# Kernel tuning notes

Hardware: AMD Instinct MI355X
Metric: run time of the kernel (lower is better)

Reference implementation:

```python
import jax, jax.numpy as jnp
import numpy as np
import math

# dims: batch, tgt len, enc len, embed, heads, layers, ffn, vocab, text dim, image dim, gate hidden
B, T, S, E, H, L, F, V, DT, DI, GH = 16, 200, 100, 256, 8, 2, 1024, 50000, 768, 512, 64
NEG = -1e9

PARAM_SHAPES = [
    ("item_emb", (V, E)), ("pos_emb", (T, E)),
    ("sa_qkv_w", (L, E, 3 * E)), ("sa_qkv_b", (L, 3 * E)), ("sa_out_w", (L, E, E)), ("sa_out_b", (L, E)),
    ("ca_qkv_w", (L, E, 3 * E)), ("ca_qkv_b", (L, 3 * E)), ("ca_out_w", (L, E, E)), ("ca_out_b", (L, E)),
    ("n1_s", (L, E)), ("n1_b", (L, E)), ("n2_s", (L, E)), ("n2_b", (L, E)), ("n3_s", (L, E)), ("n3_b", (L, E)),
    ("ffn_w1", (L, E, F)), ("ffn_b1", (L, F)), ("ffn_w2", (L, F, E)), ("ffn_b2", (L, E)),
    ("g_w1", (E, GH)), ("g_b1", (GH,)), ("g_w2", (GH, 3)), ("g_b2", (3,)),
    ("be_w", (E, E)), ("be_b", (E,)),
    ("text_mat", (V, DT)), ("tp_w", (DT, E)), ("tp_b", (E,)),
    ("ct_qkv_w", (E, 3 * E)), ("ct_qkv_b", (3 * E,)), ("ct_out_w", (E, E)), ("ct_out_b", (E,)),
    ("ce_w1", (E, 2 * E)), ("ce_b1", (2 * E,)), ("ce_w2", (2 * E, E)), ("ce_b2", (E,)),
    ("img_mat", (V, DI)), ("ip_w", (DI, E)), ("ip_b", (E,)),
    ("im_qkv_w", (E, 3 * E)), ("im_qkv_b", (3 * E,)), ("im_out_w", (E, E)), ("im_out_b", (E,)),
    ("ie_w1", (E, 2 * E)), ("ie_b1", (2 * E,)), ("ie_w2", (2 * E, E)), ("ie_b2", (E,)),
    ("fin_w", (E, V)), ("fin_b", (V,)),
]


def setup_inputs() -> dict:
    keys = iter(jax.random.split(jax.random.key(0), 80))
    d = {}
    d["target_ids"] = jax.random.randint(next(keys), (B, T), 0, V)
    d["encoder_output"] = jax.random.normal(next(keys), (B, S, E), dtype=jnp.float32)
    d["memory_padding_mask"] = jax.random.randint(next(keys), (B, S), 0, 2) == 1
    for name, shape in PARAM_SHAPES:
        d[name] = jax.random.normal(next(keys), shape, dtype=jnp.float32) * 0.02
    for n in ("n1_s", "n2_s", "n3_s"):
        d[n] = jnp.ones((L, E), jnp.float32)  # LayerNorm gains init to 1
    d["item_emb"] = d["item_emb"].at[0].set(0.0)  # padding_idx=0
    return d


def _ln(x, s, b, eps=1e-5):
    mu = jnp.mean(x, axis=-1, keepdims=True)
    var = jnp.mean(jnp.square(x - mu), axis=-1, keepdims=True)
    return (x - mu) / jnp.sqrt(var + eps) * s + b


def _mha(xq, xkv, wqkv, bqkv, wout, bout, bias):
    # torch nn.MultiheadAttention (batch_first): joint QKV proj, H heads, out proj
    Bq, Tq, _ = xq.shape
    Tk = xkv.shape[1]
    wq, wk, wv = jnp.split(wqkv, 3, axis=1)
    bq, bk, bv = jnp.split(bqkv, 3)
    Dh = E // H
    q = (xq @ wq + bq).reshape(Bq, Tq, H, Dh)
    k = (xkv @ wk + bk).reshape(Bq, Tk, H, Dh)
    v = (xkv @ wv + bv).reshape(Bq, Tk, H, Dh)
    logits = jnp.einsum("bthd,bshd->bhts", q, k) / math.sqrt(Dh)
    if bias is not None:
        logits = logits + bias
    a = jax.nn.softmax(logits, axis=-1)
    ctx = jnp.einsum("bhts,bshd->bthd", a, v).reshape(Bq, Tq, E)
    return ctx @ wout + bout


def reference(target_ids, encoder_output, memory_padding_mask, item_emb, pos_emb,
              sa_qkv_w, sa_qkv_b, sa_out_w, sa_out_b, ca_qkv_w, ca_qkv_b, ca_out_w, ca_out_b,
              n1_s, n1_b, n2_s, n2_b, n3_s, n3_b, ffn_w1, ffn_b1, ffn_w2, ffn_b2,
              g_w1, g_b1, g_w2, g_b2, be_w, be_b,
              text_mat, tp_w, tp_b, ct_qkv_w, ct_qkv_b, ct_out_w, ct_out_b, ce_w1, ce_b1, ce_w2, ce_b2,
              img_mat, ip_w, ip_b, im_qkv_w, im_qkv_b, im_out_w, im_out_b, ie_w1, ie_b1, ie_w2, ie_b2,
              fin_w, fin_b):
    causal = jnp.where(jnp.tril(jnp.ones((T, T), bool)), 0.0, -jnp.inf)[None, None]  # [1,1,T,T]
    pad_bias = jnp.where(memory_padding_mask[:, None, None, :], NEG, 0.0)  # [B,1,1,S]
    x = item_emb[target_ids] * math.sqrt(E) + pos_emb[None]  # [B,T,E]
    for l in range(L):
        x = _ln(x + _mha(x, x, sa_qkv_w[l], sa_qkv_b[l], sa_out_w[l], sa_out_b[l], causal), n1_s[l], n1_b[l])
        x = _ln(x + _mha(x, encoder_output, ca_qkv_w[l], ca_qkv_b[l], ca_out_w[l], ca_out_b[l], pad_bias), n2_s[l], n2_b[l])
        h = jax.nn.relu(x @ ffn_w1[l] + ffn_b1[l]) @ ffn_w2[l] + ffn_b2[l]
        x = _ln(x + h, n3_s[l], n3_b[l])
    # softmax gate over 3 experts (eval: no noise)
    gate = jax.nn.softmax(jax.nn.relu(x @ g_w1 + g_b1) @ g_w2 + g_b2, axis=-1)  # [B,T,3]
    e_beh = x @ be_w + be_b
    th = text_mat[target_ids] @ tp_w + tp_b
    cctx = _mha(x, th, ct_qkv_w, ct_qkv_b, ct_out_w, ct_out_b, None)
    e_txt = jax.nn.relu(cctx @ ce_w1 + ce_b1) @ ce_w2 + ce_b2
    ih = img_mat[target_ids] @ ip_w + ip_b
    ictx = _mha(x, ih, im_qkv_w, im_qkv_b, im_out_w, im_out_b, None)
    e_img = jax.nn.relu(ictx @ ie_w1 + ie_b1) @ ie_w2 + ie_b2
    hfin = gate[..., 0:1] * e_beh + gate[..., 1:2] * e_txt + gate[..., 2:3] * e_img  # [B,T,E]
    return hfin @ fin_w + fin_b  # [B,T,V] full-vocab logits
```

## Files before the change

### kernel.cpp

```cpp
#include <hip/hip_runtime.h>
#include <cstdint>
#include <cstddef>

#define BB 16
#define TT 200
#define SS 100
#define EE 256
#define HH 8
#define LL 2
#define FF 1024
#define VV 50000
#define DTXT 768
#define DIMG 512
#define GHH 64
#define MROWS (BB * TT)
#define MENC  (BB * SS)

using bf16x8 = __attribute__((ext_vector_type(8))) short;
using f32x4  = __attribute__((ext_vector_type(4))) float;

__device__ __forceinline__ short f2bf(float f) {
    unsigned u = __float_as_uint(f);
    u += 0x7fffu + ((u >> 16) & 1u);
    return (short)(u >> 16);
}

__global__ __launch_bounds__(256)
void k_transpose_bf16(const float* __restrict__ in, short* __restrict__ out, int K, int N) {
    __shared__ float tile[32][33];
    int n0 = blockIdx.x * 32, k0 = blockIdx.y * 32;
    for (int i = threadIdx.y; i < 32; i += 8) {
        int k = k0 + i, n = n0 + threadIdx.x;
        tile[i][threadIdx.x] = (k < K && n < N) ? in[(size_t)k * N + n] : 0.f;
    }
    __syncthreads();
    for (int i = threadIdx.y; i < 32; i += 8) {
        int n = n0 + i, k = k0 + threadIdx.x;
        if (n < N && k < K) out[(size_t)n * K + k] = f2bf(tile[threadIdx.x][i]);
    }
}

__global__ __launch_bounds__(256)
void k_gemm_bf16(const float* __restrict__ A, int lda, const int* __restrict__ aidx,
                 const short* __restrict__ Bt, const float* __restrict__ bias,
                 float* __restrict__ C, int ldc, int M, int N, int K, int dorelu) {
    int tid  = threadIdx.x;
    int wave = tid >> 6, lane = tid & 63;
    int lr = lane & 15, lq = lane >> 4;
    int m_base = blockIdx.y * 128 + (wave >> 1) * 64;
    int n_base = blockIdx.x * 128 + (wave & 1) * 64;

    const float* arow[4];
    const short* brow[4];
#pragma unroll
    for (int mt = 0; mt < 4; ++mt) {
        int m = m_base + mt * 16 + lr;
        if (m >= M) m = M - 1;
        int r = aidx ? aidx[m] : m;
        arow[mt] = A + (size_t)r * lda + lq * 8;
    }
#pragma unroll
    for (int nt = 0; nt < 4; ++nt) {
        int n = n_base + nt * 16 + lr;
        if (n >= N) n = N - 1;
        brow[nt] = Bt + (size_t)n * K + lq * 8;
    }

    f32x4 acc[4][4];
#pragma unroll
    for (int a = 0; a < 4; ++a)
#pragma unroll
        for (int b = 0; b < 4; ++b)
#pragma unroll
            for (int i = 0; i < 4; ++i) acc[a][b][i] = 0.f;

    for (int k0 = 0; k0 < K; k0 += 32) {
        bf16x8 af[4], bfr[4];
#pragma unroll
        for (int mt = 0; mt < 4; ++mt) {
            const float4* p = (const float4*)(arow[mt] + k0);
            float4 u = p[0], v = p[1];
            bf16x8 t;
            t[0] = f2bf(u.x); t[1] = f2bf(u.y); t[2] = f2bf(u.z); t[3] = f2bf(u.w);
            t[4] = f2bf(v.x); t[5] = f2bf(v.y); t[6] = f2bf(v.z); t[7] = f2bf(v.w);
            af[mt] = t;
        }
#pragma unroll
        for (int nt = 0; nt < 4; ++nt)
            bfr[nt] = *(const bf16x8*)(brow[nt] + k0);
#pragma unroll
        for (int mt = 0; mt < 4; ++mt)
#pragma unroll
            for (int nt = 0; nt < 4; ++nt)
                acc[mt][nt] = __builtin_amdgcn_mfma_f32_16x16x32_bf16(af[mt], bfr[nt], acc[mt][nt], 0, 0, 0);
    }

#pragma unroll
    for (int mt = 0; mt < 4; ++mt)
#pragma unroll
        for (int nt = 0; nt < 4; ++nt) {
            int col = n_base + nt * 16 + lr;
            if (col >= N) continue;
            float bv = bias ? bias[col] : 0.f;
#pragma unroll
            for (int i = 0; i < 4; ++i) {
                int row = m_base + mt * 16 + lq * 4 + i;
                if (row >= M) continue;
                float v = acc[mt][nt][i] + bv;
                if (dorelu) v = fmaxf(v, 0.f);
                C[(size_t)row * ldc + col] = v;
            }
        }
}

template <int MODE>
__global__ __launch_bounds__(256)
void k_attn(const float* __restrict__ q, int qld,
            const float* __restrict__ k, const float* __restrict__ v, int kvld,
            const int* __restrict__ mask,
            float* __restrict__ out, int T, int Tk) {
    int b = blockIdx.z, h = blockIdx.y;
    int t = threadIdx.x;
    __shared__ float kl[TT][32];
    __shared__ float vl[TT][32];
    for (int idx = threadIdx.x; idx < Tk * 32; idx += 256) {
        int s = idx >> 5, i = idx & 31;
        kl[s][i] = k[((size_t)b * Tk + s) * kvld + h * 32 + i];
        vl[s][i] = v[((size_t)b * Tk + s) * kvld + h * 32 + i];
    }
    __syncthreads();
    if (t >= T) return;

    float qv[32];
    const float* qp = q + ((size_t)b * T + t) * qld + h * 32;
#pragma unroll
    for (int i = 0; i < 32; ++i) qv[i] = qp[i];

    float m = -INFINITY, l = 0.f, ctx[32];
#pragma unroll
    for (int i = 0; i < 32; ++i) ctx[i] = 0.f;

    int send = (MODE == 1) ? (t + 1) : Tk;
    for (int s = 0; s < send; ++s) {
        float d = 0.f;
#pragma unroll
        for (int i = 0; i < 32; ++i) d += qv[i] * kl[s][i];
        d *= 0.17677669529663687f;
        if (MODE == 2) { if (mask[b * Tk + s]) d += -1e9f; }
        if (d > m) {
            float f = __expf(m - d);
            l *= f;
#pragma unroll
            for (int i = 0; i < 32; ++i) ctx[i] *= f;
            m = d;
        }
        float p = __expf(d - m);
        l += p;
#pragma unroll
        for (int i = 0; i < 32; ++i) ctx[i] += p * vl[s][i];
    }
    float inv = 1.f / l;
    float* op = out + ((size_t)b * T + t) * EE + h * 32;
#pragma unroll
    for (int i = 0; i < 32; ++i) op[i] = ctx[i] * inv;
}

__global__ __launch_bounds__(256)
void k_ln_res(const float* __restrict__ a, const float* __restrict__ bres,
              const float* __restrict__ gain, const float* __restrict__ beta,
              float* __restrict__ out) {
    int row = blockIdx.x, i = threadIdx.x;
    __shared__ float red[256];
    float x = a[(size_t)row * EE + i] + bres[(size_t)row * EE + i];
    red[i] = x;
    __syncthreads();
    for (int s = 128; s > 0; s >>= 1) { if (i < s) red[i] += red[i + s]; __syncthreads(); }
    float mu = red[0] * (1.f / EE);
    __syncthreads();
    float d = x - mu;
    red[i] = d * d;
    __syncthreads();
    for (int s = 128; s > 0; s >>= 1) { if (i < s) red[i] += red[i + s]; __syncthreads(); }
    float var = red[0] * (1.f / EE);
    float r = rsqrtf(var + 1e-5f);
    out[(size_t)row * EE + i] = d * r * gain[i] + beta[i];
}

__global__ __launch_bounds__(64)
void k_gate(const float* __restrict__ x, const float* __restrict__ w1, const float* __restrict__ b1,
            const float* __restrict__ w2, const float* __restrict__ b2, float* __restrict__ gate) {
    int row = blockIdx.x, j = threadIdx.x;
    __shared__ float xr[EE];
    __shared__ float hr[GHH];
    for (int i = j; i < EE; i += 64) xr[i] = x[(size_t)row * EE + i];
    __syncthreads();
    float acc = b1[j];
    for (int i = 0; i < EE; ++i) acc += xr[i] * w1[i * GHH + j];
    hr[j] = fmaxf(acc, 0.f);
    __syncthreads();
    if (j == 0) {
        float g[3];
        for (int c = 0; c < 3; ++c) {
            float a = b2[c];
            for (int kk = 0; kk < GHH; ++kk) a += hr[kk] * w2[kk * 3 + c];
            g[c] = a;
        }
        float mx = fmaxf(g[0], fmaxf(g[1], g[2]));
        float e0 = __expf(g[0] - mx), e1 = __expf(g[1] - mx), e2 = __expf(g[2] - mx);
        float inv = 1.f / (e0 + e1 + e2);
        gate[(size_t)row * 3 + 0] = e0 * inv;
        gate[(size_t)row * 3 + 1] = e1 * inv;
        gate[(size_t)row * 3 + 2] = e2 * inv;
    }
}

__global__ __launch_bounds__(256)
void k_embed(const int* __restrict__ ids, const float* __restrict__ item,
             const float* __restrict__ pos, float* __restrict__ out) {
    int idx = blockIdx.x * 256 + threadIdx.x;
    if (idx >= MROWS * EE) return;
    int bt = idx >> 8, e = idx & 255;
    int t = bt % TT;
    out[idx] = item[(size_t)ids[bt] * EE + e] * 16.f + pos[t * EE + e];
}

__global__ __launch_bounds__(256)
void k_combine(const float* __restrict__ g, const float* __restrict__ e0,
               const float* __restrict__ e1, const float* __restrict__ e2,
               float* __restrict__ out) {
    int idx = blockIdx.x * 256 + threadIdx.x;
    if (idx >= MROWS * EE) return;
    int row = idx >> 8;
    out[idx] = g[(size_t)row * 3] * e0[idx] + g[(size_t)row * 3 + 1] * e1[idx] + g[(size_t)row * 3 + 2] * e2[idx];
}

extern "C" void kernel_launch(void* const* d_in, const int* in_sizes, int n_in,
                              void* d_out, int out_size, void* d_ws, size_t ws_size,
                              hipStream_t stream) {
    (void)in_sizes; (void)n_in; (void)out_size; (void)ws_size;

    const int*   ids      = (const int*)d_in[0];
    const float* enc      = (const float*)d_in[1];
    const int*   mask     = (const int*)d_in[2];
    const float* item_emb = (const float*)d_in[3];
    const float* pos_emb  = (const float*)d_in[4];
    const float* sa_qkv_w = (const float*)d_in[5];
    const float* sa_qkv_b = (const float*)d_in[6];
    const float* sa_out_w = (const float*)d_in[7];
    const float* sa_out_b = (const float*)d_in[8];
    const float* ca_qkv_w = (const float*)d_in[9];
    const float* ca_qkv_b = (const float*)d_in[10];
    const float* ca_out_w = (const float*)d_in[11];
    const float* ca_out_b = (const float*)d_in[12];
    const float* n1_s = (const float*)d_in[13];
    const float* n1_b = (const float*)d_in[14];
    const float* n2_s = (const float*)d_in[15];
    const float* n2_b = (const float*)d_in[16];
    const float* n3_s = (const float*)d_in[17];
    const float* n3_b = (const float*)d_in[18];
    const float* ffn_w1 = (const float*)d_in[19];
    const float* ffn_b1 = (const float*)d_in[20];
    const float* ffn_w2 = (const float*)d_in[21];
    const float* ffn_b2 = (const float*)d_in[22];
    const float* g_w1 = (const float*)d_in[23];
    const float* g_b1 = (const float*)d_in[24];
    const float* g_w2 = (const float*)d_in[25];
    const float* g_b2 = (const float*)d_in[26];
    const float* be_w = (const float*)d_in[27];
    const float* be_b = (const float*)d_in[28];
    const float* text_mat = (const float*)d_in[29];
    const float* tp_w = (const float*)d_in[30];
    const float* tp_b = (const float*)d_in[31];
    const float* ct_qkv_w = (const float*)d_in[32];
    const float* ct_qkv_b = (const float*)d_in[33];
    const float* ct_out_w = (const float*)d_in[34];
    const float* ct_out_b = (const float*)d_in[35];
    const float* ce_w1 = (const float*)d_in[36];
    const float* ce_b1 = (const float*)d_in[37];
    const float* ce_w2 = (const float*)d_in[38];
    const float* ce_b2 = (const float*)d_in[39];
    const float* img_mat = (const float*)d_in[40];
    const float* ip_w = (const float*)d_in[41];
    const float* ip_b = (const float*)d_in[42];
    const float* im_qkv_w = (const float*)d_in[43];
    const float* im_qkv_b = (const float*)d_in[44];
    const float* im_out_w = (const float*)d_in[45];
    const float* im_out_b = (const float*)d_in[46];
    const float* ie_w1 = (const float*)d_in[47];
    const float* ie_b1 = (const float*)d_in[48];
    const float* ie_w2 = (const float*)d_in[49];
    const float* ie_b2 = (const float*)d_in[50];
    const float* fin_w = (const float*)d_in[51];
    const float* fin_b = (const float*)d_in[52];
    float* out = (float*)d_out;

    char* pws = (char*)d_ws;
    auto alloc = [&](size_t bytes) -> void* {
        void* r = (void*)pws;
        pws += (bytes + 255) & ~(size_t)255;
        return r;
    };
    short* wsaqkv = (short*)alloc((size_t)LL * 768 * 256 * 2);
    short* wsaout = (short*)alloc((size_t)LL * 256 * 256 * 2);
    short* wcaqkv = (short*)alloc((size_t)LL * 768 * 256 * 2);
    short* wcaout = (short*)alloc((size_t)LL * 256 * 256 * 2);
    short* wffn1  = (short*)alloc((size_t)LL * 1024 * 256 * 2);
    short* wffn2  = (short*)alloc((size_t)LL * 256 * 1024 * 2);
    short* wbe    = (short*)alloc((size_t)256 * 256 * 2);
    short* wtp    = (short*)alloc((size_t)256 * 768 * 2);
    short* wctqkv = (short*)alloc((size_t)768 * 256 * 2);
    short* wctout = (short*)alloc((size_t)256 * 256 * 2);
    short* wce1   = (short*)alloc((size_t)512 * 256 * 2);
    short* wce2   = (short*)alloc((size_t)256 * 512 * 2);
    short* wip    = (short*)alloc((size_t)256 * 512 * 2);
    short* wimqkv = (short*)alloc((size_t)768 * 256 * 2);
    short* wimout = (short*)alloc((size_t)256 * 256 * 2);
    short* wie1   = (short*)alloc((size_t)512 * 256 * 2);
    short* wie2   = (short*)alloc((size_t)256 * 512 * 2);
    short* wfin   = (short*)alloc((size_t)VV * 256 * 2);

    float* xbuf   = (float*)alloc((size_t)MROWS * 256 * 4);
    float* qkvbuf = (float*)alloc((size_t)MROWS * 768 * 4);
    float* qbuf   = (float*)alloc((size_t)MROWS * 256 * 4);
    float* kvbuf  = (float*)alloc((size_t)MROWS * 512 * 4);
    float* ctxbuf = (float*)alloc((size_t)MROWS * 256 * 4);
    float* obuf   = (float*)alloc((size_t)MROWS * 256 * 4);
    float* pbuf   = (float*)alloc((size_t)MROWS * 1024 * 4);
    float* thbuf  = (float*)alloc((size_t)MROWS * 256 * 4);
    float* gatebuf= (float*)alloc((size_t)MROWS * 4 * 4);
    float* ebeh   = (float*)alloc((size_t)MROWS * 256 * 4);
    float* etxt   = (float*)alloc((size_t)MROWS * 256 * 4);
    float* eimg   = (float*)alloc((size_t)MROWS * 256 * 4);
    float* hfin   = (float*)alloc((size_t)MROWS * 256 * 4);

    auto tr = [&](const float* in, short* o, int K, int N) {
        dim3 g((N + 31) / 32, (K + 31) / 32);
        k_transpose_bf16<<<g, dim3(32, 8), 0, stream>>>(in, o, K, N);
    };
    auto gemm = [&](const float* A, int lda, const int* aidx, const short* Bt,
                    const float* bias, float* C, int ldc, int M, int N, int K, int relu) {
        dim3 g((N + 127) / 128, (M + 127) / 128);
        k_gemm_bf16<<<g, 256, 0, stream>>>(A, lda, aidx, Bt, bias, C, ldc, M, N, K, relu);
    };
    auto attn = [&](int mode, const float* q, int qld, const float* k, const float* v,
                    int kvld, const int* mk, float* o, int Tk) {
        dim3 g(1, HH, BB);
        if (mode == 0)      k_attn<0><<<g, 256, 0, stream>>>(q, qld, k, v, kvld, mk, o, TT, Tk);
        else if (mode == 1) k_attn<1><<<g, 256, 0, stream>>>(q, qld, k, v, kvld, mk, o, TT, Tk);
        else                k_attn<2><<<g, 256, 0, stream>>>(q, qld, k, v, kvld, mk, o, TT, Tk);
    };
    auto ln = [&](const float* a, const float* b, const float* gain, const float* beta, float* o) {
        k_ln_res<<<MROWS, 256, 0, stream>>>(a, b, gain, beta, o);
    };

    for (int l = 0; l < LL; ++l) {
        tr(sa_qkv_w + (size_t)l * 256 * 768, wsaqkv + (size_t)l * 768 * 256, 256, 768);
        tr(sa_out_w + (size_t)l * 256 * 256, wsaout + (size_t)l * 256 * 256, 256, 256);
        tr(ca_qkv_w + (size_t)l * 256 * 768, wcaqkv + (size_t)l * 768 * 256, 256, 768);
        tr(ca_out_w + (size_t)l * 256 * 256, wcaout + (size_t)l * 256 * 256, 256, 256);
        tr(ffn_w1 + (size_t)l * 256 * 1024, wffn1 + (size_t)l * 1024 * 256, 256, 1024);
        tr(ffn_w2 + (size_t)l * 1024 * 256, wffn2 + (size_t)l * 256 * 1024, 1024, 256);
    }
    tr(be_w, wbe, 256, 256);
    tr(tp_w, wtp, 768, 256);
    tr(ct_qkv_w, wctqkv, 256, 768);
    tr(ct_out_w, wctout, 256, 256);
    tr(ce_w1, wce1, 256, 512);
    tr(ce_w2, wce2, 512, 256);
    tr(ip_w, wip, 512, 256);
    tr(im_qkv_w, wimqkv, 256, 768);
    tr(im_out_w, wimout, 256, 256);
    tr(ie_w1, wie1, 256, 512);
    tr(ie_w2, wie2, 512, 256);
    tr(fin_w, wfin, 256, VV);

    k_embed<<<(MROWS * EE + 255) / 256, 256, 0, stream>>>(ids, item_emb, pos_emb, xbuf);

    for (int l = 0; l < LL; ++l) {
        gemm(xbuf, 256, nullptr, wsaqkv + (size_t)l * 768 * 256, sa_qkv_b + (size_t)l * 768,
             qkvbuf, 768, MROWS, 768, 256, 0);
        attn(1, qkvbuf, 768, qkvbuf + 256, qkvbuf + 512, 768, nullptr, ctxbuf, TT);
        gemm(ctxbuf, 256, nullptr, wsaout + (size_t)l * 256 * 256, sa_out_b + (size_t)l * 256,
             obuf, 256, MROWS, 256, 256, 0);
        ln(xbuf, obuf, n1_s + (size_t)l * 256, n1_b + (size_t)l * 256, xbuf);
        gemm(xbuf, 256, nullptr, wcaqkv + (size_t)l * 768 * 256, ca_qkv_b + (size_t)l * 768,
             qbuf, 256, MROWS, 256, 256, 0);
        gemm(enc, 256, nullptr, wcaqkv + (size_t)l * 768 * 256 + 256 * 256,
             ca_qkv_b + (size_t)l * 768 + 256, kvbuf, 512, MENC, 512, 256, 0);
        attn(2, qbuf, 256, kvbuf, kvbuf + 256, 512, mask, ctxbuf, SS);
        gemm(ctxbuf, 256, nullptr, wcaout + (size_t)l * 256 * 256, ca_out_b + (size_t)l * 256,
             obuf, 256, MROWS, 256, 256, 0);
        ln(xbuf, obuf, n2_s + (size_t)l * 256, n2_b + (size_t)l * 256, xbuf);
        gemm(xbuf, 256, nullptr, wffn1 + (size_t)l * 1024 * 256, ffn_b1 + (size_t)l * 1024,
             pbuf, 1024, MROWS, 1024, 256, 1);
        gemm(pbuf, 1024, nullptr, wffn2 + (size_t)l * 256 * 1024, ffn_b2 + (size_t)l * 256,
             obuf, 256, MROWS, 256, 1024, 0);
        ln(xbuf, obuf, n3_s + (size_t)l * 256, n3_b + (size_t)l * 256, xbuf);
    }

    k_gate<<<MROWS, 64, 0, stream>>>(xbuf, g_w1, g_b1, g_w2, g_b2, gatebuf);
    gemm(xbuf, 256, nullptr, wbe, be_b, ebeh, 256, MROWS, 256, 256, 0);

    gemm(text_mat, DTXT, ids, wtp, tp_b, thbuf, 256, MROWS, 256, DTXT, 0);
    gemm(xbuf, 256, nullptr, wctqkv, ct_qkv_b, qbuf, 256, MROWS, 256, 256, 0);
    gemm(thbuf, 256, nullptr, wctqkv + 256 * 256, ct_qkv_b + 256, kvbuf, 512, MROWS, 512, 256, 0);
    attn(0, qbuf, 256, kvbuf, kvbuf + 256, 512, nullptr, ctxbuf, TT);
    gemm(ctxbuf, 256, nullptr, wctout, ct_out_b, obuf, 256, MROWS, 256, 256, 0);
    gemm(obuf, 256, nullptr, wce1, ce_b1, pbuf, 512, MROWS, 512, 256, 1);
    gemm(pbuf, 512, nullptr, wce2, ce_b2, etxt, 256, MROWS, 256, 512, 0);

    gemm(img_mat, DIMG, ids, wip, ip_b, thbuf, 256, MROWS, 256, DIMG, 0);
    gemm(xbuf, 256, nullptr, wimqkv, im_qkv_b, qbuf, 256, MROWS, 256, 256, 0);
    gemm(thbuf, 256, nullptr, wimqkv + 256 * 256, im_qkv_b + 256, kvbuf, 512, MROWS, 512, 256, 0);
    attn(0, qbuf, 256, kvbuf, kvbuf + 256, 512, nullptr, ctxbuf, TT);
    gemm(ctxbuf, 256, nullptr, wimout, im_out_b, obuf, 256, MROWS, 256, 256, 0);
    gemm(obuf, 256, nullptr, wie1, ie_b1, pbuf, 512, MROWS, 512, 256, 1);
    gemm(pbuf, 512, nullptr, wie2, ie_b2, eimg, 256, MROWS, 256, 512, 0);

    k_combine<<<(MROWS * EE + 255) / 256, 256, 0, stream>>>(gatebuf, ebeh, etxt, eimg, hfin);
    gemm(hfin, 256, nullptr, wfin, fin_b, out, VV, MROWS, VV, 256, 0);
}
```

Measured before the change: 2.544 ms.

## Stage bf16 GEMM operands through LDS with double-buffered direct loads

Rewrites the GEMM to take bf16 A operands and stage 128x64 A/B tiles into LDS with global_load_lds, double-buffered across K steps. Producers (layernorm, embed, attention, combine, GEMM epilogues) now emit bf16 copies, and the encoder, text and image gathers are pre-cast to bf16 rows. The aim is to cut global traffic and the fp32->bf16 conversion inside the GEMM inner loop, and to overlap loads with MFMA. The cost is extra bf16 buffers and cast kernels, and intermediates are rounded to bf16. The loop assumes K is a multiple of 64.

```diff
diff --git a/kernel.cpp b/kernel.cpp
--- a/kernel.cpp
+++ b/kernel.cpp
@@ -41,30 +41,60 @@
 }
 
 __global__ __launch_bounds__(256)
-void k_gemm_bf16(const float* __restrict__ A, int lda, const int* __restrict__ aidx,
-                 const short* __restrict__ Bt, const float* __restrict__ bias,
-                 float* __restrict__ C, int ldc, int M, int N, int K, int dorelu) {
+void k_cast_rows(const float* __restrict__ in, int ldin, const int* __restrict__ idx,
+                 short* __restrict__ out, int cols) {
+    int r = blockIdx.x;
+    int src = idx ? idx[r] : r;
+    const float4* ip = (const float4*)(in + (size_t)src * ldin);
+    short* op = out + (size_t)r * cols;
+    for (int j = threadIdx.x; j * 4 < cols; j += blockDim.x) {
+        float4 u = ip[j];
+        short4 s;
+        s.x = f2bf(u.x); s.y = f2bf(u.y); s.z = f2bf(u.z); s.w = f2bf(u.w);
+        *(short4*)(op + j * 4) = s;
+    }
+}
+
+__global__ __launch_bounds__(256, 2)
+void k_gemm_bf16(const short* __restrict__ A, int lda,
+                 const short* __restrict__ Bt, int ldb,
+                 const float* __restrict__ bias,
+                 float* __restrict__ C, short* __restrict__ Cb, int ldc,
+                 int M, int N, int K, int dorelu) {
+    __shared__ short lsa[2][8][128][8];
+    __shared__ short lsb[2][8][128][8];
     int tid  = threadIdx.x;
     int wave = tid >> 6, lane = tid & 63;
     int lr = lane & 15, lq = lane >> 4;
-    int m_base = blockIdx.y * 128 + (wave >> 1) * 64;
-    int n_base = blockIdx.x * 128 + (wave & 1) * 64;
-
-    const float* arow[4];
-    const short* brow[4];
-#pragma unroll
-    for (int mt = 0; mt < 4; ++mt) {
-        int m = m_base + mt * 16 + lr;
-        if (m >= M) m = M - 1;
-        int r = aidx ? aidx[m] : m;
-        arow[mt] = A + (size_t)r * lda + lq * 8;
-    }
-#pragma unroll
-    for (int nt = 0; nt < 4; ++nt) {
-        int n = n_base + nt * 16 + lr;
-        if (n >= N) n = N - 1;
-        brow[nt] = Bt + (size_t)n * K + lq * 8;
-    }
+    int wm = (wave >> 1) * 64, wn = (wave & 1) * 64;
+    int mblk = blockIdx.y * 128, nblk = blockIdx.x * 128;
+
+    const short* pA[4];
+    const short* pB[4];
+#pragma unroll
+    for (int i = 0; i < 4; ++i) {
+        int c = wave * 4 + i;
+        int kg = c >> 1, half = (c & 1) * 64;
+        int ra = mblk + half + lane; if (ra > M - 1) ra = M - 1;
+        int rb = nblk + half + lane; if (rb > N - 1) rb = N - 1;
+        pA[i] = A  + (size_t)ra * lda + kg * 8;
+        pB[i] = Bt + (size_t)rb * ldb + kg * 8;
+    }
+
+    auto stage = [&](int buf) {
+#pragma unroll
+        for (int i = 0; i < 4; ++i) {
+            int c = wave * 4 + i;
+            int kg = c >> 1, half = (c & 1) * 64;
+            __builtin_amdgcn_global_load_lds(
+                (const __attribute__((address_space(1))) void*)pA[i],
+                (__attribute__((address_space(3))) void*)&lsa[buf][kg][half][0], 16, 0, 0);
+            __builtin_amdgcn_global_load_lds(
+                (const __attribute__((address_space(1))) void*)pB[i],
+                (__attribute__((address_space(3))) void*)&lsb[buf][kg][half][0], 16, 0, 0);
+            pA[i] += 64; pB[i] += 64;
+        }
+    };
 
     f32x4 acc[4][4];
 #pragma unroll
@@ -74,41 +104,47 @@
 #pragma unroll
             for (int i = 0; i < 4; ++i) acc[a][b][i] = 0.f;
 
-    for (int k0 = 0; k0 < K; k0 += 32) {
-        bf16x8 af[4], bfr[4];
-#pragma unroll
-        for (int mt = 0; mt < 4; ++mt) {
-            const float4* p = (const float4*)(arow[mt] + k0);
-            float4 u = p[0], v = p[1];
-            bf16x8 t;
-            t[0] = f2bf(u.x); t[1] = f2bf(u.y); t[2] = f2bf(u.z); t[3] = f2bf(u.w);
-            t[4] = f2bf(v.x); t[5] = f2bf(v.y); t[6] = f2bf(v.z); t[7] = f2bf(v.w);
-            af[mt] = t;
-        }
-#pragma unroll
-        for (int nt = 0; nt < 4; ++nt)
-            bfr[nt] = *(const bf16x8*)(brow[nt] + k0);
-#pragma unroll
-        for (int mt = 0; mt < 4; ++mt)
-#pragma unroll
-            for (int nt = 0; nt < 4; ++nt)
-                acc[mt][nt] = __builtin_amdgcn_mfma_f32_16x16x32_bf16(af[mt], bfr[nt], acc[mt][nt], 0, 0, 0);
+    stage(0);
+    __syncthreads();
+
+    int nk = K >> 6;
+    for (int kt = 0; kt < nk; ++kt) {
+        int cur = kt & 1;
+        if (kt + 1 < nk) stage(cur ^ 1);
+        bf16x8 af[2][4], bfr[2][4];
+#pragma unroll
+        for (int kk = 0; kk < 2; ++kk)
+#pragma unroll
+            for (int t = 0; t < 4; ++t) {
+                af[kk][t]  = *(const bf16x8*)&lsa[cur][kk * 4 + lq][wm + t * 16 + lr][0];
+                bfr[kk][t] = *(const bf16x8*)&lsb[cur][kk * 4 + lq][wn + t * 16 + lr][0];
+            }
+#pragma unroll
+        for (int kk = 0; kk < 2; ++kk)
+#pragma unroll
+            for (int mt = 0; mt < 4; ++mt)
+#pragma unroll
+                for (int nt = 0; nt < 4; ++nt)
+                    acc[mt][nt] = __builtin_amdgcn_mfma_f32_16x16x32_bf16(
+                        af[kk][mt], bfr[kk][nt], acc[mt][nt], 0, 0, 0);
+        __syncthreads();
     }
 
 #pragma unroll
     for (int mt = 0; mt < 4; ++mt)
 #pragma unroll
         for (int nt = 0; nt < 4; ++nt) {
-            int col = n_base + nt * 16 + lr;
+            int col = nblk + wn + nt * 16 + lr;
             if (col >= N) continue;
             float bv = bias ? bias[col] : 0.f;
 #pragma unroll
             for (int i = 0; i < 4; ++i) {
-                int row = m_base + mt * 16 + lq * 4 + i;
+                int row = mblk + wm + mt * 16 + lq * 4 + i;
                 if (row >= M) continue;
                 float v = acc[mt][nt][i] + bv;
                 if (dorelu) v = fmaxf(v, 0.f);
-                C[(size_t)row * ldc + col] = v;
+                if (C)  C[(size_t)row * ldc + col]  = v;
+                if (Cb) Cb[(size_t)row * ldc + col] = f2bf(v);
             }
         }
 }
@@ -118,7 +154,7 @@
 void k_attn(const float* __restrict__ q, int qld,
             const float* __restrict__ k, const float* __restrict__ v, int kvld,
             const int* __restrict__ mask,
-            float* __restrict__ out, int T, int Tk) {
+            short* __restrict__ out, int T, int Tk) {
     int b = blockIdx.z, h = blockIdx.y;
     int t = threadIdx.x;
     __shared__ float kl[TT][32];
@@ -160,15 +196,15 @@
         for (int i = 0; i < 32; ++i) ctx[i] += p * vl[s][i];
     }
     float inv = 1.f / l;
-    float* op = out + ((size_t)b * T + t) * EE + h * 32;
-#pragma unroll
-    for (int i = 0; i < 32; ++i) op[i] = ctx[i] * inv;
+    short* op = out + ((size_t)b * T + t) * EE + h * 32;
+#pragma unroll
+    for (int i = 0; i < 32; ++i) op[i] = f2bf(ctx[i] * inv);
 }
 
 __global__ __launch_bounds__(256)
 void k_ln_res(const float* __restrict__ a, const float* __restrict__ bres,
               const float* __restrict__ gain, const float* __restrict__ beta,
-              float* __restrict__ out) {
+              float* __restrict__ out, short* __restrict__ ob) {
     int row = blockIdx.x, i = threadIdx.x;
     __shared__ float red[256];
     float x = a[(size_t)row * EE + i] + bres[(size_t)row * EE + i];
@@ -183,7 +219,9 @@
     for (int s = 128; s > 0; s >>= 1) { if (i < s) red[i] += red[i + s]; __syncthreads(); }
     float var = red[0] * (1.f / EE);
     float r = rsqrtf(var + 1e-5f);
-    out[(size_t)row * EE + i] = d * r * gain[i] + beta[i];
+    float y = d * r * gain[i] + beta[i];
+    out[(size_t)row * EE + i] = y;
+    ob[(size_t)row * EE + i] = f2bf(y);
 }
 
 __global__ __launch_bounds__(64)
@@ -216,22 +254,26 @@
 
 __global__ __launch_bounds__(256)
 void k_embed(const int* __restrict__ ids, const float* __restrict__ item,
-             const float* __restrict__ pos, float* __restrict__ out) {
+             const float* __restrict__ pos, float* __restrict__ out,
+             short* __restrict__ xb) {
     int idx = blockIdx.x * 256 + threadIdx.x;
     if (idx >= MROWS * EE) return;
     int bt = idx >> 8, e = idx & 255;
     int t = bt % TT;
-    out[idx] = item[(size_t)ids[bt] * EE + e] * 16.f + pos[t * EE + e];
+    float v = item[(size_t)ids[bt] * EE + e] * 16.f + pos[t * EE + e];
+    out[idx] = v;
+    xb[idx] = f2bf(v);
 }
 
 __global__ __launch_bounds__(256)
 void k_combine(const float* __restrict__ g, const float* __restrict__ e0,
                const float* __restrict__ e1, const float* __restrict__ e2,
-               float* __restrict__ out) {
+               short* __restrict__ out) {
     int idx = blockIdx.x * 256 + threadIdx.x;
     if (idx >= MROWS * EE) return;
     int row = idx >> 8;
-    out[idx] = g[(size_t)row * 3] * e0[idx] + g[(size_t)row * 3 + 1] * e1[idx] + g[(size_t)row * 3 + 2] * e2[idx];
+    float v = g[(size_t)row * 3] * e0[idx] + g[(size_t)row * 3 + 1] * e1[idx] + g[(size_t)row * 3 + 2] * e2[idx];
+    out[idx] = f2bf(v);
 }
 
 extern "C" void kernel_launch(void* const* d_in, const int* in_sizes, int n_in,
@@ -323,34 +365,40 @@
     float* qkvbuf = (float*)alloc((size_t)MROWS * 768 * 4);
     float* qbuf   = (float*)alloc((size_t)MROWS * 256 * 4);
     float* kvbuf  = (float*)alloc((size_t)MROWS * 512 * 4);
-    float* ctxbuf = (float*)alloc((size_t)MROWS * 256 * 4);
     float* obuf   = (float*)alloc((size_t)MROWS * 256 * 4);
-    float* pbuf   = (float*)alloc((size_t)MROWS * 1024 * 4);
-    float* thbuf  = (float*)alloc((size_t)MROWS * 256 * 4);
     float* gatebuf= (float*)alloc((size_t)MROWS * 4 * 4);
     float* ebeh   = (float*)alloc((size_t)MROWS * 256 * 4);
     float* etxt   = (float*)alloc((size_t)MROWS * 256 * 4);
     float* eimg   = (float*)alloc((size_t)MROWS * 256 * 4);
-    float* hfin   = (float*)alloc((size_t)MROWS * 256 * 4);
+    short* xb     = (short*)alloc((size_t)MROWS * 256 * 2);
+    short* encb   = (short*)alloc((size_t)MENC * 256 * 2);
+    short* ctxb   = (short*)alloc((size_t)MROWS * 256 * 2);
+    short* pbh    = (short*)alloc((size_t)MROWS * 1024 * 2);
+    short* thb    = (short*)alloc((size_t)MROWS * 256 * 2);
+    short* obb    = (short*)alloc((size_t)MROWS * 256 * 2);
+    short* hfb    = (short*)alloc((size_t)MROWS * 256 * 2);
+    short* tg     = (short*)alloc((size_t)MROWS * 768 * 2);
+    short* ig     = (short*)alloc((size_t)MROWS * 512 * 2);
 
     auto tr = [&](const float* in, short* o, int K, int N) {
         dim3 g((N + 31) / 32, (K + 31) / 32);
         k_transpose_bf16<<<g, dim3(32, 8), 0, stream>>>(in, o, K, N);
     };
-    auto gemm = [&](const float* A, int lda, const int* aidx, const short* Bt,
-                    const float* bias, float* C, int ldc, int M, int N, int K, int relu) {
+    auto gemm = [&](const short* A, int lda, const short* Bt, const float* bias,
+                    float* C, short* Cb, int ldc, int M, int N, int K, int relu) {
         dim3 g((N + 127) / 128, (M + 127) / 128);
-        k_gemm_bf16<<<g, 256, 0, stream>>>(A, lda, aidx, Bt, bias, C, ldc, M, N, K, relu);
+        k_gemm_bf16<<<g, 256, 0, stream>>>(A, lda, Bt, K, bias, C, Cb, ldc, M, N, K, relu);
     };
     auto attn = [&](int mode, const float* q, int qld, const float* k, const float* v,
-                    int kvld, const int* mk, float* o, int Tk) {
+                    int kvld, const int* mk, short* o, int Tk) {
         dim3 g(1, HH, BB);
         if (mode == 0)      k_attn<0><<<g, 256, 0, stream>>>(q, qld, k, v, kvld, mk, o, TT, Tk);
         else if (mode == 1) k_attn<1><<<g, 256, 0, stream>>>(q, qld, k, v, kvld, mk, o, TT, Tk);
         else                k_attn<2><<<g, 256, 0, stream>>>(q, qld, k, v, kvld, mk, o, TT, Tk);
     };
-    auto ln = [&](const float* a, const float* b, const float* gain, const float* beta, float* o) {
-        k_ln_res<<<MROWS, 256, 0, stream>>>(a, b, gain, beta, o);
+    auto ln = [&](const float* a, const float* b, const float* gain, const float* beta,
+                  float* o, short* ob) {
+        k_ln_res<<<MROWS, 256, 0, stream>>>(a, b, gain, beta, o, ob);
     };
 
     for (int l = 0; l < LL; ++l) {
@@ -374,49 +422,53 @@
     tr(ie_w2, wie2, 512, 256);
     tr(fin_w, wfin, 256, VV);
 
-    k_embed<<<(MROWS * EE + 255) / 256, 256, 0, stream>>>(ids, item_emb, pos_emb, xbuf);
+    k_cast_rows<<<MENC, 64, 0, stream>>>(enc, 256, nullptr, encb, 256);
+    k_cast_rows<<<MROWS, 192, 0, stream>>>(text_mat, DTXT, ids, tg, DTXT);
+    k_cast_rows<<<MROWS, 128, 0, stream>>>(img_mat, DIMG, ids, ig, DIMG);
+
+    k_embed<<<(MROWS * EE + 255) / 256, 256, 0, stream>>>(ids, item_emb, pos_emb, xbuf, xb);
 
     for (int l = 0; l < LL; ++l) {
-        gemm(xbuf, 256, nullptr, wsaqkv + (size_t)l * 768 * 256, sa_qkv_b + (size_t)l * 768,
-             qkvbuf, 768, MROWS, 768, 256, 0);
-        attn(1, qkvbuf, 768, qkvbuf + 256, qkvbuf + 512, 768, nullptr, ctxbuf, TT);
-        gemm(ctxbuf, 256, nullptr, wsaout + (size_t)l * 256 * 256, sa_out_b + (size_t)l * 256,
-             obuf, 256, MROWS, 256, 256, 0);
-        ln(xbuf, obuf, n1_s + (size_t)l * 256, n1_b + (size_t)l * 256, xbuf);
-        gemm(xbuf, 256, nullptr, wcaqkv + (size_t)l * 768 * 256, ca_qkv_b + (size_t)l * 768,
-             qbuf, 256, MROWS, 256, 256, 0);
-        gemm(enc, 256, nullptr, wcaqkv + (size_t)l * 768 * 256 + 256 * 256,
-             ca_qkv_b + (size_t)l * 768 + 256, kvbuf, 512, MENC, 512, 256, 0);
-        attn(2, qbuf, 256, kvbuf, kvbuf + 256, 512, mask, ctxbuf, SS);
-        gemm(ctxbuf, 256, nullptr, wcaout + (size_t)l * 256 * 256, ca_out_b + (size_t)l * 256,
-             obuf, 256, MROWS, 256, 256, 0);
-        ln(xbuf, obuf, n2_s + (size_t)l * 256, n2_b + (size_t)l * 256, xbuf);
-        gemm(xbuf, 256, nullptr, wffn1 + (size_t)l * 1024 * 256, ffn_b1 + (size_t)l * 1024,
-             pbuf, 1024, MROWS, 1024, 256, 1);
-        gemm(pbuf, 1024, nullptr, wffn2 + (size_t)l * 256 * 1024, ffn_b2 + (size_t)l * 256,
-             obuf, 256, MROWS, 256, 1024, 0);
-        ln(xbuf, obuf, n3_s + (size_t)l * 256, n3_b + (size_t)l * 256, xbuf);
+        gemm(xb, 256, wsaqkv + (size_t)l * 768 * 256, sa_qkv_b + (size_t)l * 768,
+             qkvbuf, nullptr, 768, MROWS, 768, 256, 0);
+        attn(1, qkvbuf, 768, qkvbuf + 256, qkvbuf + 512, 768, nullptr, ctxb, TT);
+        gemm(ctxb, 256, wsaout + (size_t)l * 256 * 256, sa_out_b + (size_t)l * 256,
+             obuf, nullptr, 256, MROWS, 256, 256, 0);
+        ln(xbuf, obuf, n1_s + (size_t)l * 256, n1_b + (size_t)l * 256, xbuf, xb);
+        gemm(xb, 256, wcaqkv + (size_t)l * 768 * 256, ca_qkv_b + (size_t)l * 768,
+             qbuf, nullptr, 256, MROWS, 256, 256, 0);
+        gemm(encb, 256, wcaqkv + (size_t)l * 768 * 256 + 256 * 256,
+             ca_qkv_b + (size_t)l * 768 + 256, kvbuf, nullptr, 512, MENC, 512, 256, 0);
+        attn(2, qbuf, 256, kvbuf, kvbuf + 256, 512, mask, ctxb, SS);
+        gemm(ctxb, 256, wcaout + (size_t)l * 256 * 256, ca_out_b + (size_t)l * 256,
+             obuf, nullptr, 256, MROWS, 256, 256, 0);
+        ln(xbuf, obuf, n2_s + (size_t)l * 256, n2_b + (size_t)l * 256, xbuf, xb);
+        gemm(xb, 256, wffn1 + (size_t)l * 1024 * 256, ffn_b1 + (size_t)l * 1024,
+             nullptr, pbh, 1024, MROWS, 1024, 256, 1);
+        gemm(pbh, 1024, wffn2 + (size_t)l * 256 * 1024, ffn_b2 + (size_t)l * 256,
+             obuf, nullptr, 256, MROWS, 256, 1024, 0);
+        ln(xbuf, obuf, n3_s + (size_t)l * 256, n3_b + (size_t)l * 256, xbuf, xb);
     }
 
     k_gate<<<MROWS, 64, 0, stream>>>(xbuf, g_w1, g_b1, g_w2, g_b2, gatebuf);
-    gemm(xbuf, 256, nullptr, wbe, be_b, ebeh, 256, MROWS, 256, 256, 0);
-
-    gemm(text_mat, DTXT, ids, wtp, tp_b, thbuf, 256, MROWS, 256, DTXT, 0);
-    gemm(xbuf, 256, nullptr, wctqkv, ct_qkv_b, qbuf, 256, MROWS, 256, 256, 0);
-    gemm(thbuf, 256, nullptr, wctqkv + 256 * 256, ct_qkv_b + 256, kvbuf, 512, MROWS, 512, 256, 0);
-    attn(0, qbuf, 256, kvbuf, kvbuf + 256, 512, nullptr, ctxbuf, TT);
-    gemm(ctxbuf, 256, nullptr, wctout, ct_out_b, obuf, 256, MROWS, 256, 256, 0);
-    gemm(obuf, 256, nullptr, wce1, ce_b1, pbuf, 512, MROWS, 512, 256, 1);
-    gemm(pbuf, 512, nullptr, wce2, ce_b2, etxt, 256, MROWS, 256, 512, 0);
-
-    gemm(img_mat, DIMG, ids, wip, ip_b, thbuf, 256, MROWS, 256, DIMG, 0);
-    gemm(xbuf, 256, nullptr, wimqkv, im_qkv_b, qbuf, 256, MROWS, 256, 256, 0);
-    gemm(thbuf, 256, nullptr, wimqkv + 256 * 256, im_qkv_b + 256, kvbuf, 512, MROWS, 512, 256, 0);
-    attn(0, qbuf, 256, kvbuf, kvbuf + 256, 512, nullptr, ctxbuf, TT);
-    gemm(ctxbuf, 256, nullptr, wimout, im_out_b, obuf, 256, MROWS, 256, 256, 0);
-    gemm(obuf, 256, nullptr, wie1, ie_b1, pbuf, 512, MROWS, 512, 256, 1);
-    gemm(pbuf, 512, nullptr, wie2, ie_b2, eimg, 256, MROWS, 256, 512, 0);
-
-    k_combine<<<(MROWS * EE + 255) / 256, 256, 0, stream>>>(gatebuf, ebeh, etxt, eimg, hfin);
-    gemm(hfin, 256, nullptr, wfin, fin_b, out, VV, MROWS, VV, 256, 0);
-}
+    gemm(xb, 256, wbe, be_b, ebeh, nullptr, 256, MROWS, 256, 256, 0);
+
+    gemm(tg, DTXT, wtp, tp_b, nullptr, thb, 256, MROWS, 256, DTXT, 0);
+    gemm(xb, 256, wctqkv, ct_qkv_b, qbuf, nullptr, 256, MROWS, 256, 256, 0);
+    gemm(thb, 256, wctqkv + 256 * 256, ct_qkv_b + 256, kvbuf, nullptr, 512, MROWS, 512, 256, 0);
+    attn(0, qbuf, 256, kvbuf, kvbuf + 256, 512, nullptr, ctxb, TT);
+    gemm(ctxb, 256, wctout, ct_out_b, nullptr, obb, 256, MROWS, 256, 256, 0);
+    gemm(obb, 256, wce1, ce_b1, nullptr, pbh, 512, MROWS, 512, 256, 1);
+    gemm(pbh, 512, wce2, ce_b2, etxt, nullptr, 256, MROWS, 256, 512, 0);
+
+    gemm(ig, DIMG, wip, ip_b, nullptr, thb, 256, MROWS, 256, DIMG, 0);
+    gemm(xb, 256, wimqkv, im_qkv_b, qbuf, nullptr, 256, MROWS, 256, 256, 0);
+    gemm(thb, 256, wimqkv + 256 * 256, im_qkv_b + 256, kvbuf, nullptr, 512, MROWS, 512, 256, 0);
+    attn(0, qbuf, 256, kvbuf, kvbuf + 256, 512, nullptr, ctxb, TT);
+    gemm(ctxb, 256, wimout, im_out_b, nullptr, obb, 256, MROWS, 256, 256, 0);
+    gemm(obb, 256, wie1, ie_b1, nullptr, pbh, 512, MROWS, 512, 256, 1);
+    gemm(pbh, 512, wie2, ie_b2, eimg, nullptr, 256, MROWS, 256, 512, 0);
+
+    k_combine<<<(MROWS * EE + 255) / 256, 256, 0, stream>>>(gatebuf, ebeh, etxt, eimg, hfb);
+    gemm(hfb, 256, wfin, fin_b, out, nullptr, VV, MROWS, VV, 256, 0);
+}
```

Result: faster. 2.251 ms (-11.5%).
